# Kernel optimization log

Measured on AMD Instinct MI355X. Metric: run time of the kernel, lower is better.

## Reference

```python
import jax, jax.numpy as jnp
import numpy as np

B, S, D, H = 2, 2048, 1024, 16
DH = D // H          # 64
SP = S // 2          # projected kv length (Linformer)
SCALE = float(np.sqrt(DH))


def setup_inputs() -> dict:
    key = jax.random.key(0)
    ks = jax.random.split(key, 20)
    std = 0.02
    inp = {
        "query": jax.random.normal(ks[0], (B, S, D), jnp.float32),
        "key": jax.random.normal(ks[1], (B, S, D), jnp.float32),
        "value": jax.random.normal(ks[2], (B, S, D), jnp.float32),
        "mask": jax.random.randint(ks[3], (B, 1, 1, S), 0, 2, jnp.int32),
        "Wq": jax.random.normal(ks[4], (D, D), jnp.float32) * std,
        "bq": jnp.zeros((D,), jnp.float32),
        "Wk": jax.random.normal(ks[5], (D, D), jnp.float32) * std,
        "bk": jnp.zeros((D,), jnp.float32),
        "Wv": jax.random.normal(ks[6], (D, D), jnp.float32) * std,
        "bv": jnp.zeros((D,), jnp.float32),
        "Wo": jax.random.normal(ks[7], (D, D), jnp.float32) * std,
        "bo": jnp.zeros((D,), jnp.float32),
        "WkP": jax.random.normal(ks[8], (SP, S), jnp.float32) * std,
        "bkP": jnp.zeros((SP,), jnp.float32),
        "WvP": jax.random.normal(ks[9], (SP, S), jnp.float32) * std,
        "bvP": jnp.zeros((SP,), jnp.float32),
        "apply_proj": 1,
    }
    return inp


def reference(query, key, value, mask, Wq, bq, Wk, bk, Wv, bv, Wo, bo,
              WkP, bkP, WvP, bvP, apply_proj):
    # lin_forward path (apply_proj=True); dropout_ratio=0 -> dropout is identity.
    def heads(x, W, b):  # [B,S,D] -> [B,H,S,DH]
        return (x @ W.T + b).reshape(B, S, H, DH).transpose(0, 2, 1, 3)

    Q = heads(query, Wq, bq)
    K = heads(key, Wk, bk)
    V = heads(value, Wv, bv)

    # masked_fill on transposed [B,H,DH,S] == zero out seq positions
    mseq = (mask != 0).astype(Q.dtype).transpose(0, 1, 3, 2)  # [B,1,S,1]
    Q, K, V = Q * mseq, K * mseq, V * mseq

    # Linformer seq projection S -> SP with exact GELU ('nonlin' config)
    Kp = jax.nn.gelu(jnp.einsum('bhsd,ps->bhpd', K, WkP)
                     + bkP[None, None, :, None], approximate=False)
    Vp = jax.nn.gelu(jnp.einsum('bhsd,ps->bhpd', V, WvP)
                     + bvP[None, None, :, None], approximate=False)

    score = jnp.einsum('bhsd,bhpd->bhsp', Q, Kp) / SCALE   # [B,H,S,SP]
    attn = jax.nn.softmax(score, axis=-1)
    x = jnp.einsum('bhsp,bhpd->bhsd', attn, Vp)            # [B,H,S,DH]
    x = x.transpose(0, 2, 1, 3).reshape(B, S, D)
    return x @ Wo.T + bo
```

## Files before the change

kernel.cpp:

```cpp
#include <hip/hip_runtime.h>
#include <hip/hip_bf16.h>


typedef __attribute__((ext_vector_type(4))) float  f32x4;
typedef __attribute__((ext_vector_type(8))) short  short8;
typedef __attribute__((ext_vector_type(4))) short  short4_t;
typedef __attribute__((ext_vector_type(2))) unsigned int uint32x2;
typedef __attribute__((ext_vector_type(8))) __bf16 bf16x8;
typedef unsigned short ushort_t;

#define DEV __device__ __forceinline__

constexpr int B_ = 2, S_ = 2048, D_ = 1024, H_ = 16, SP_ = 1024;
constexpr size_t M1 = 1u << 20;
constexpr size_t XQ_OFF = 0,      XK_OFF = 4*M1,  XV_OFF = 8*M1,
                 WQ_OFF = 12*M1,  WK_OFF = 13*M1, WV_OFF = 14*M1, WO_OFF = 15*M1,
                 QB_OFF = 4*M1,   KP_OFF = 0,     VPT_OFF = 2*M1,
                 WKPB_OFF = 8*M1, WVPB_OFF = 10*M1, XO_OFF = 8*M1;

DEV ushort_t f2bf(float f) {
  unsigned u = __builtin_bit_cast(unsigned, f);
  unsigned r = ((u >> 16) & 1u) + 0x7FFFu;
  return (ushort_t)((u + r) >> 16);
}
DEV bf16x8 ld8(const ushort_t* p) {
  return __builtin_bit_cast(bf16x8, *reinterpret_cast<const short8*>(p));
}
DEV f32x4 mfma16(bf16x8 a, bf16x8 b, f32x4 c) {
  return __builtin_amdgcn_mfma_f32_16x16x32_bf16(a, b, c, 0, 0, 0);
}
DEV void gload16(const ushort_t* g, ushort_t* l) {
  __builtin_amdgcn_global_load_lds(
      (const __attribute__((address_space(1))) void*)g,
      (__attribute__((address_space(3))) void*)l, 16, 0, 0);
}
DEV void cvt2048(const float* src, ushort_t* dst, int tid) {
  const size_t off = (size_t)tid * 8;
  float4 f0 = *reinterpret_cast<const float4*>(src + off);
  float4 f1 = *reinterpret_cast<const float4*>(src + off + 4);
  ushort_t t[8] = { f2bf(f0.x), f2bf(f0.y), f2bf(f0.z), f2bf(f0.w),
                    f2bf(f1.x), f2bf(f1.y), f2bf(f1.z), f2bf(f1.w) };
  *reinterpret_cast<short8*>(dst + off) = *reinterpret_cast<short8*>(t);
}

__global__ __launch_bounds__(256) void k_convert_a(
    const float* __restrict__ q, const float* __restrict__ k,
    const float* __restrict__ v, const float* __restrict__ Wq,
    const float* __restrict__ Wk, const float* __restrict__ Wv,
    const float* __restrict__ Wo, ushort_t* __restrict__ ws)
{
  int blk = blockIdx.x; const float* src; ushort_t* dst;
  if      (blk < 2048) { src = q;  dst = ws + XQ_OFF; }
  else if (blk < 4096) { src = k;  dst = ws + XK_OFF; blk -= 2048; }
  else if (blk < 6144) { src = v;  dst = ws + XV_OFF; blk -= 4096; }
  else if (blk < 6656) { src = Wq; dst = ws + WQ_OFF; blk -= 6144; }
  else if (blk < 7168) { src = Wk; dst = ws + WK_OFF; blk -= 6656; }
  else if (blk < 7680) { src = Wv; dst = ws + WV_OFF; blk -= 7168; }
  else                 { src = Wo; dst = ws + WO_OFF; blk -= 7680; }
  cvt2048(src + (size_t)blk * 2048, dst + (size_t)blk * 2048, threadIdx.x);
}

__global__ __launch_bounds__(256) void k_convert_b(
    const float* __restrict__ WkP, const float* __restrict__ WvP,
    ushort_t* __restrict__ ws)
{
  int blk = blockIdx.x; const float* src; ushort_t* dst;
  if (blk < 1024) { src = WkP; dst = ws + WKPB_OFF; }
  else            { src = WvP; dst = ws + WVPB_OFF; blk -= 1024; }
  cvt2048(src + (size_t)blk * 2048, dst + (size_t)blk * 2048, threadIdx.x);
}

template<int BIAS, int EPI, int OUTMODE>
DEV void gemmT(const ushort_t* Ap, const ushort_t* Bp, const float* bias,
               const int* mask, void* Cp, int M, int N, int K)
{
  __shared__ __align__(16) ushort_t As[64 * 64];
  __shared__ __align__(16) ushort_t Bs[128 * 64];
  const int tid = threadIdx.x;

  const int gx = gridDim.x, gy = gridDim.y, nwg = gx * gy;
  int lin = blockIdx.y * gx + blockIdx.x;
  lin = (lin & 7) * (nwg >> 3) + (lin >> 3);
  const int m0 = (lin / gy) * 64, n0 = (lin % gy) * 128;

  const int w = tid >> 6, lane = tid & 63, lr = lane & 15, lg = lane >> 4;
  const int wm = (w >> 1) * 32, wn = (w & 1) * 64;
  const int rk7 = lr & 7;

  f32x4 acc[2][4];
#pragma unroll
  for (int i = 0; i < 2; ++i)
#pragma unroll
    for (int j = 0; j < 4; ++j) acc[i][j] = f32x4{0.f, 0.f, 0.f, 0.f};

  const int srow = tid >> 3;
  const int schx = ((tid & 7) ^ (srow & 7)) * 8;
  const ushort_t* Ag = Ap + (size_t)(m0 + srow) * K + schx;
  const ushort_t* Bg = Bp + (size_t)(n0 + srow) * K + schx;

  for (int k0 = 0; k0 < K; k0 += 64) {
    gload16(Ag + k0,                 As + tid*8);
    gload16(Ag + (size_t)32*K + k0,  As + 2048 + tid*8);
    gload16(Bg + k0,                 Bs + tid*8);
    gload16(Bg + (size_t)32*K + k0,  Bs + 2048 + tid*8);
    gload16(Bg + (size_t)64*K + k0,  Bs + 4096 + tid*8);
    gload16(Bg + (size_t)96*K + k0,  Bs + 6144 + tid*8);
    __syncthreads();

#pragma unroll
    for (int ks = 0; ks < 2; ++ks) {
      bf16x8 af[2], bfv[4];
#pragma unroll
      for (int i = 0; i < 2; ++i)
        af[i]  = ld8(&As[(wm + i*16 + lr)*64 + (((ks<<2)|lg) ^ rk7)*8]);
#pragma unroll
      for (int j = 0; j < 4; ++j)
        bfv[j] = ld8(&Bs[(wn + j*16 + lr)*64 + (((ks<<2)|lg) ^ rk7)*8]);
#pragma unroll
      for (int i = 0; i < 2; ++i)
#pragma unroll
        for (int j = 0; j < 4; ++j)
          acc[i][j] = mfma16(af[i], bfv[j], acc[i][j]);
    }
    __syncthreads();
  }

#pragma unroll
  for (int i = 0; i < 2; ++i) {
    const int mBase = m0 + wm + i*16 + 4*lg;
#pragma unroll
    for (int j = 0; j < 4; ++j) {
      const int n = n0 + wn + j*16 + lr;
      float vv[4];
#pragma unroll
      for (int r = 0; r < 4; ++r) {
        const int m = mBase + r;
        float v = acc[i][j][r];
        if (BIAS == 2) v += bias[n];
        if (BIAS == 1) v += bias[m];
        if (EPI == 1)  v = mask[m] ? v : 0.f;
        if (EPI == 2)  v = 0.5f * v * (1.f + erff(v * 0.70710678118654752f));
        vv[r] = v;
      }
      if (OUTMODE == 0) {
#pragma unroll
        for (int r = 0; r < 4; ++r)
          ((ushort_t*)Cp)[(size_t)(mBase + r) * N + n] = f2bf(vv[r]);
      } else if (OUTMODE == 1) {
#pragma unroll
        for (int r = 0; r < 4; ++r)
          ((float*)Cp)[(size_t)(mBase + r) * N + n] = vv[r];
      } else if (OUTMODE == 2) {
        const int bb = mBase >> 11;
        const int sb = mBase & (S_ - 1);
        ushort_t t4[4] = { f2bf(vv[0]), f2bf(vv[1]), f2bf(vv[2]), f2bf(vv[3]) };
        *reinterpret_cast<short4_t*>(
            (ushort_t*)Cp + ((size_t)bb * D_ + n) * S_ + sb) =
            *reinterpret_cast<short4_t*>(t4);
      } else {
        ushort_t t4[4] = { f2bf(vv[0]), f2bf(vv[1]), f2bf(vv[2]), f2bf(vv[3]) };
        *reinterpret_cast<short4_t*>(
            (ushort_t*)Cp + (size_t)n * M + mBase) =
            *reinterpret_cast<short4_t*>(t4);
      }
    }
  }
}

__global__ __launch_bounds__(256) void k_kv(
    const float* __restrict__ bk, const float* __restrict__ bv,
    const int* __restrict__ mask, const ushort_t* __restrict__ ws,
    ushort_t* __restrict__ KbT, ushort_t* __restrict__ VbT)
{
  if (blockIdx.z == 0)
    gemmT<2, 1, 2>(ws + XK_OFF, ws + WK_OFF, bk, mask, KbT, B_*S_, D_, D_);
  else
    gemmT<2, 1, 2>(ws + XV_OFF, ws + WV_OFF, bv, mask, VbT, B_*S_, D_, D_);
}

__global__ __launch_bounds__(256) void k_q(
    const float* __restrict__ bq, const int* __restrict__ mask,
    const ushort_t* __restrict__ ws, ushort_t* __restrict__ Qb)
{
  gemmT<2, 1, 0>(ws + XQ_OFF, ws + WQ_OFF, bq, mask, Qb, B_*S_, D_, D_);
}

__global__ __launch_bounds__(256) void k_linproj(
    const float* __restrict__ bkP, const float* __restrict__ bvP,
    const ushort_t* __restrict__ ws, const ushort_t* __restrict__ KbT,
    const ushort_t* __restrict__ VbT, ushort_t* __restrict__ Kp,
    ushort_t* __restrict__ VpT)
{
  const int z = blockIdx.z, b = z >> 1, isv = z & 1;
  if (isv) {
    gemmT<1, 2, 3>(ws + WVPB_OFF, VbT + (size_t)b * D_ * S_, bvP,
                   nullptr, VpT + (size_t)b * D_ * SP_, SP_, D_, S_);
  } else {
    gemmT<1, 2, 0>(ws + WKPB_OFF, KbT + (size_t)b * D_ * S_, bkP,
                   nullptr, Kp + (size_t)b * SP_ * D_, SP_, D_, S_);
  }
}

__global__ __launch_bounds__(256) void k_outproj(
    const ushort_t* __restrict__ Xo, const ushort_t* __restrict__ Wob,
    const float* __restrict__ bo, float* __restrict__ out)
{
  gemmT<2, 0, 1>(Xo, Wob, bo, nullptr, out, B_*S_, D_, D_);
}

__global__ __launch_bounds__(512) void attn_kernel(
    const ushort_t* __restrict__ Qb, const ushort_t* __restrict__ Kp,
    const ushort_t* __restrict__ VpT, ushort_t* __restrict__ Xo)
{
  __shared__ __align__(16) ushort_t Ks[2][64 * 64];
  __shared__ __align__(16) ushort_t Vs[2][64 * 64];
  __shared__ __align__(16) ushort_t Pl[8][16][72];

  const int b = blockIdx.z, h = blockIdx.y, s0 = blockIdx.x * 128;
  const int tid = threadIdx.x, w = tid >> 6, lane = tid & 63;
  const int lr = lane & 15, lg = lane >> 4;

  const ushort_t* qp = Qb + (size_t)(b * S_ + s0 + w*16 + lr) * D_ + h * 64;
  const bf16x8 aq0 = ld8(qp + 8*lg);
  const bf16x8 aq1 = ld8(qp + 32 + 8*lg);

  const ushort_t* kbase = Kp  + (size_t)b * SP_ * D_ + h * 64;
  const ushort_t* vbase = VpT + (size_t)b * D_ * SP_ + (size_t)(h*64) * SP_;

  const int srow = tid >> 3, sch = tid & 7;
  const int schx = (sch ^ (srow & 7)) << 3;

  f32x4 o[4];
#pragma unroll
  for (int dt = 0; dt < 4; ++dt) o[dt] = f32x4{0.f, 0.f, 0.f, 0.f};
  float lsum4[4] = {0.f, 0.f, 0.f, 0.f};
  constexpr float C_ = 0.18033688011112042f;

  gload16(kbase + (size_t)srow * D_ + schx, Ks[0] + tid*8);
  gload16(vbase + (size_t)srow * SP_ + schx, Vs[0] + tid*8);
  __syncthreads();

  int cur = 0;
  for (int pt = 0; pt < SP_ / 64; ++pt) {
    if (pt + 1 < SP_ / 64) {
      const int p1 = (pt + 1) * 64;
      gload16(kbase + (size_t)(p1 + srow) * D_ + schx, Ks[cur^1] + tid*8);
      gload16(vbase + (size_t)srow * SP_ + p1 + schx, Vs[cur^1] + tid*8);
    }

    const int rk7 = lr & 7;
#pragma unroll
    for (int nt = 0; nt < 4; ++nt) {
      const ushort_t* krow = Ks[cur] + (nt*16 + lr) * 64;
      f32x4 a = f32x4{0.f, 0.f, 0.f, 0.f};
      a = mfma16(ld8(krow + ((lg       ^ rk7) << 3)), aq0, a);
      a = mfma16(ld8(krow + (((4 + lg) ^ rk7) << 3)), aq1, a);
      const float e0 = __builtin_exp2f(a[0] * C_);
      const float e1 = __builtin_exp2f(a[1] * C_);
      const float e2 = __builtin_exp2f(a[2] * C_);
      const float e3 = __builtin_exp2f(a[3] * C_);
      lsum4[nt] += (e0 + e1) + (e2 + e3);
      unsigned p01, p23;
      asm("v_cvt_pk_bf16_f32 %0, %1, %2" : "=v"(p01) : "v"(e0), "v"(e1));
      asm("v_cvt_pk_bf16_f32 %0, %1, %2" : "=v"(p23) : "v"(e2), "v"(e3));
      uint32x2 pw; pw[0] = p01; pw[1] = p23;
      *reinterpret_cast<uint32x2*>(&Pl[w][lr][nt*16 + 4*lg]) = pw;
    }

    const bf16x8 pa0 = ld8(&Pl[w][lr][8*lg]);
    const bf16x8 pa1 = ld8(&Pl[w][lr][32 + 8*lg]);
#pragma unroll
    for (int dt = 0; dt < 4; ++dt) {
      const ushort_t* vrow = Vs[cur] + (dt*16 + lr) * 64;
      o[dt] = mfma16(pa0, ld8(vrow + ((lg       ^ rk7) << 3)), o[dt]);
      o[dt] = mfma16(pa1, ld8(vrow + (((4 + lg) ^ rk7) << 3)), o[dt]);
    }

    __syncthreads();
    cur ^= 1;
  }

  float lsum = (lsum4[0] + lsum4[1]) + (lsum4[2] + lsum4[3]);
  lsum += __shfl_xor(lsum, 16, 64);
  lsum += __shfl_xor(lsum, 32, 64);
  float linv[4];
#pragma unroll
  for (int r = 0; r < 4; ++r)
    linv[r] = 1.f / __shfl(lsum, 4*lg + r, 64);

#pragma unroll
  for (int dt = 0; dt < 4; ++dt)
#pragma unroll
    for (int r = 0; r < 4; ++r) {
      const int srow2 = s0 + w*16 + 4*lg + r;
      Xo[(size_t)(b * S_ + srow2) * D_ + h*64 + dt*16 + lr] =
          f2bf(o[dt][r] * linv[r]);
    }
}

extern "C" void kernel_launch(void* const* d_in, const int* in_sizes, int n_in,
                              void* d_out, int out_size, void* d_ws, size_t ws_size,
                              hipStream_t stream)
{
  const float* q   = (const float*)d_in[0];
  const float* k   = (const float*)d_in[1];
  const float* v   = (const float*)d_in[2];
  const int*   msk = (const int*)d_in[3];
  const float* Wq  = (const float*)d_in[4];
  const float* bq  = (const float*)d_in[5];
  const float* Wk  = (const float*)d_in[6];
  const float* bk  = (const float*)d_in[7];
  const float* Wv  = (const float*)d_in[8];
  const float* bv  = (const float*)d_in[9];
  const float* Wo  = (const float*)d_in[10];
  const float* bo  = (const float*)d_in[11];
  const float* WkP = (const float*)d_in[12];
  const float* bkP = (const float*)d_in[13];
  const float* WvP = (const float*)d_in[14];
  const float* bvP = (const float*)d_in[15];

  ushort_t* ws  = (ushort_t*)d_ws;
  ushort_t* Qb  = ws + QB_OFF;
  ushort_t* Kp  = ws + KP_OFF;
  ushort_t* VpT = ws + VPT_OFF;
  ushort_t* Xo  = ws + XO_OFF;
  ushort_t* KbT = (ushort_t*)d_out;
  ushort_t* VbT = KbT + 4 * M1;

  dim3 blk(256, 1, 1);
  k_convert_a<<<dim3(8192, 1, 1), blk, 0, stream>>>(q, k, v, Wq, Wk, Wv, Wo, ws);
  k_kv     <<<dim3(B_*S_/64, D_/128, 2), blk, 0, stream>>>(bk, bv, msk, ws, KbT, VbT);
  k_q      <<<dim3(B_*S_/64, D_/128, 1), blk, 0, stream>>>(bq, msk, ws, Qb);
  k_convert_b<<<dim3(2048, 1, 1), blk, 0, stream>>>(WkP, WvP, ws);
  k_linproj<<<dim3(SP_/64,  D_/128, 4), blk, 0, stream>>>(bkP, bvP, ws, KbT, VbT, Kp, VpT);
  attn_kernel<<<dim3(S_/128, H_, B_), dim3(512,1,1), 0, stream>>>(Qb, Kp, VpT, Xo);
  k_outproj<<<dim3(B_*S_/64, D_/128, 1), blk, 0, stream>>>(Xo, ws + WO_OFF, bo, (float*)d_out);
}
```

Before: 148.5 us.

## Process two query groups per attention block and fold softmax scale into Q

The attention kernel now handles 256 query rows per block, two 128-row groups, and loads each K/V tile's fragments from LDS once into registers for reuse by both groups. This halves K/V global loads and LDS traffic per query row. The softmax scale constant is multiplied into Q in the Q-projection epilogue, so the exp2 in the inner loop no longer needs a multiply. The costs are half as many blocks (256 vs 512), more registers per thread under a launch-bounds hint of two blocks, and Q stored in bf16 after scaling, which adds a small rounding difference.

```diff
diff --git a/kernel.cpp b/kernel.cpp
--- a/kernel.cpp
+++ b/kernel.cpp
@@ -17,6 +17,7 @@
                  WQ_OFF = 12*M1,  WK_OFF = 13*M1, WV_OFF = 14*M1, WO_OFF = 15*M1,
                  QB_OFF = 4*M1,   KP_OFF = 0,     VPT_OFF = 2*M1,
                  WKPB_OFF = 8*M1, WVPB_OFF = 10*M1, XO_OFF = 8*M1;
+constexpr float CSC = 0.18033688011112042f;
 
 DEV ushort_t f2bf(float f) {
   unsigned u = __builtin_bit_cast(unsigned, f);
@@ -138,7 +139,8 @@
         float v = acc[i][j][r];
         if (BIAS == 2) v += bias[n];
         if (BIAS == 1) v += bias[m];
-        if (EPI == 1)  v = mask[m] ? v : 0.f;
+        if (EPI == 1 || EPI == 3) v = mask[m] ? v : 0.f;
+        if (EPI == 3)  v *= CSC;
         if (EPI == 2)  v = 0.5f * v * (1.f + erff(v * 0.70710678118654752f));
         vv[r] = v;
       }
@@ -182,7 +184,7 @@
     const float* __restrict__ bq, const int* __restrict__ mask,
     const ushort_t* __restrict__ ws, ushort_t* __restrict__ Qb)
 {
-  gemmT<2, 1, 0>(ws + XQ_OFF, ws + WQ_OFF, bq, mask, Qb, B_*S_, D_, D_);
+  gemmT<2, 3, 0>(ws + XQ_OFF, ws + WQ_OFF, bq, mask, Qb, B_*S_, D_, D_);
 }
 
 __global__ __launch_bounds__(256) void k_linproj(
@@ -208,7 +210,7 @@
   gemmT<2, 0, 1>(Xo, Wob, bo, nullptr, out, B_*S_, D_, D_);
 }
 
-__global__ __launch_bounds__(512) void attn_kernel(
+__global__ __launch_bounds__(512, 2) void attn_kernel(
     const ushort_t* __restrict__ Qb, const ushort_t* __restrict__ Kp,
     const ushort_t* __restrict__ VpT, ushort_t* __restrict__ Xo)
 {
@@ -216,25 +218,32 @@
   __shared__ __align__(16) ushort_t Vs[2][64 * 64];
   __shared__ __align__(16) ushort_t Pl[8][16][72];
 
-  const int b = blockIdx.z, h = blockIdx.y, s0 = blockIdx.x * 128;
+  const int b = blockIdx.z, h = blockIdx.y, s0 = blockIdx.x * 256;
   const int tid = threadIdx.x, w = tid >> 6, lane = tid & 63;
   const int lr = lane & 15, lg = lane >> 4;
 
-  const ushort_t* qp = Qb + (size_t)(b * S_ + s0 + w*16 + lr) * D_ + h * 64;
-  const bf16x8 aq0 = ld8(qp + 8*lg);
-  const bf16x8 aq1 = ld8(qp + 32 + 8*lg);
+  bf16x8 aq[2][2];
+#pragma unroll
+  for (int g = 0; g < 2; ++g) {
+    const ushort_t* qp =
+        Qb + (size_t)(b * S_ + s0 + g*128 + w*16 + lr) * D_ + h * 64;
+    aq[g][0] = ld8(qp + 8*lg);
+    aq[g][1] = ld8(qp + 32 + 8*lg);
+  }
 
   const ushort_t* kbase = Kp  + (size_t)b * SP_ * D_ + h * 64;
   const ushort_t* vbase = VpT + (size_t)b * D_ * SP_ + (size_t)(h*64) * SP_;
 
   const int srow = tid >> 3, sch = tid & 7;
   const int schx = (sch ^ (srow & 7)) << 3;
-
-  f32x4 o[4];
-#pragma unroll
-  for (int dt = 0; dt < 4; ++dt) o[dt] = f32x4{0.f, 0.f, 0.f, 0.f};
-  float lsum4[4] = {0.f, 0.f, 0.f, 0.f};
-  constexpr float C_ = 0.18033688011112042f;
+  const int rk7 = lr & 7;
+
+  f32x4 o[2][4];
+#pragma unroll
+  for (int g = 0; g < 2; ++g)
+#pragma unroll
+    for (int dt = 0; dt < 4; ++dt) o[g][dt] = f32x4{0.f, 0.f, 0.f, 0.f};
+  float lsum4[2][4] = {};
 
   gload16(kbase + (size_t)srow * D_ + schx, Ks[0] + tid*8);
   gload16(vbase + (size_t)srow * SP_ + schx, Vs[0] + tid*8);
@@ -248,54 +257,66 @@
       gload16(vbase + (size_t)srow * SP_ + p1 + schx, Vs[cur^1] + tid*8);
     }
 
-    const int rk7 = lr & 7;
+    bf16x8 kf[4][2], vf[4][2];
 #pragma unroll
     for (int nt = 0; nt < 4; ++nt) {
       const ushort_t* krow = Ks[cur] + (nt*16 + lr) * 64;
-      f32x4 a = f32x4{0.f, 0.f, 0.f, 0.f};
-      a = mfma16(ld8(krow + ((lg       ^ rk7) << 3)), aq0, a);
-      a = mfma16(ld8(krow + (((4 + lg) ^ rk7) << 3)), aq1, a);
-      const float e0 = __builtin_exp2f(a[0] * C_);
-      const float e1 = __builtin_exp2f(a[1] * C_);
-      const float e2 = __builtin_exp2f(a[2] * C_);
-      const float e3 = __builtin_exp2f(a[3] * C_);
-      lsum4[nt] += (e0 + e1) + (e2 + e3);
-      unsigned p01, p23;
-      asm("v_cvt_pk_bf16_f32 %0, %1, %2" : "=v"(p01) : "v"(e0), "v"(e1));
-      asm("v_cvt_pk_bf16_f32 %0, %1, %2" : "=v"(p23) : "v"(e2), "v"(e3));
-      uint32x2 pw; pw[0] = p01; pw[1] = p23;
-      *reinterpret_cast<uint32x2*>(&Pl[w][lr][nt*16 + 4*lg]) = pw;
-    }
-
-    const bf16x8 pa0 = ld8(&Pl[w][lr][8*lg]);
-    const bf16x8 pa1 = ld8(&Pl[w][lr][32 + 8*lg]);
-#pragma unroll
-    for (int dt = 0; dt < 4; ++dt) {
-      const ushort_t* vrow = Vs[cur] + (dt*16 + lr) * 64;
-      o[dt] = mfma16(pa0, ld8(vrow + ((lg       ^ rk7) << 3)), o[dt]);
-      o[dt] = mfma16(pa1, ld8(vrow + (((4 + lg) ^ rk7) << 3)), o[dt]);
+      kf[nt][0] = ld8(krow + ((lg       ^ rk7) << 3));
+      kf[nt][1] = ld8(krow + (((4 + lg) ^ rk7) << 3));
+      const ushort_t* vrow = Vs[cur] + (nt*16 + lr) * 64;
+      vf[nt][0] = ld8(vrow + ((lg       ^ rk7) << 3));
+      vf[nt][1] = ld8(vrow + (((4 + lg) ^ rk7) << 3));
+    }
+
+#pragma unroll
+    for (int g = 0; g < 2; ++g) {
+#pragma unroll
+      for (int nt = 0; nt < 4; ++nt) {
+        f32x4 a = f32x4{0.f, 0.f, 0.f, 0.f};
+        a = mfma16(kf[nt][0], aq[g][0], a);
+        a = mfma16(kf[nt][1], aq[g][1], a);
+        const float e0 = __builtin_exp2f(a[0]);
+        const float e1 = __builtin_exp2f(a[1]);
+        const float e2 = __builtin_exp2f(a[2]);
+        const float e3 = __builtin_exp2f(a[3]);
+        lsum4[g][nt] += (e0 + e1) + (e2 + e3);
+        unsigned p01, p23;
+        asm("v_cvt_pk_bf16_f32 %0, %1, %2" : "=v"(p01) : "v"(e0), "v"(e1));
+        asm("v_cvt_pk_bf16_f32 %0, %1, %2" : "=v"(p23) : "v"(e2), "v"(e3));
+        uint32x2 pw; pw[0] = p01; pw[1] = p23;
+        *reinterpret_cast<uint32x2*>(&Pl[w][lr][nt*16 + 4*lg]) = pw;
+      }
+      const bf16x8 pa0 = ld8(&Pl[w][lr][8*lg]);
+      const bf16x8 pa1 = ld8(&Pl[w][lr][32 + 8*lg]);
+#pragma unroll
+      for (int dt = 0; dt < 4; ++dt) {
+        o[g][dt] = mfma16(pa0, vf[dt][0], o[g][dt]);
+        o[g][dt] = mfma16(pa1, vf[dt][1], o[g][dt]);
+      }
     }
 
     __syncthreads();
     cur ^= 1;
   }
 
-  float lsum = (lsum4[0] + lsum4[1]) + (lsum4[2] + lsum4[3]);
-  lsum += __shfl_xor(lsum, 16, 64);
-  lsum += __shfl_xor(lsum, 32, 64);
-  float linv[4];
-#pragma unroll
-  for (int r = 0; r < 4; ++r)
-    linv[r] = 1.f / __shfl(lsum, 4*lg + r, 64);
-
-#pragma unroll
-  for (int dt = 0; dt < 4; ++dt)
-#pragma unroll
-    for (int r = 0; r < 4; ++r) {
-      const int srow2 = s0 + w*16 + 4*lg + r;
-      Xo[(size_t)(b * S_ + srow2) * D_ + h*64 + dt*16 + lr] =
-          f2bf(o[dt][r] * linv[r]);
-    }
+#pragma unroll
+  for (int g = 0; g < 2; ++g) {
+    float lsum = (lsum4[g][0] + lsum4[g][1]) + (lsum4[g][2] + lsum4[g][3]);
+    lsum += __shfl_xor(lsum, 16, 64);
+    lsum += __shfl_xor(lsum, 32, 64);
+    float linv[4];
+#pragma unroll
+    for (int r = 0; r < 4; ++r)
+      linv[r] = 1.f / __shfl(lsum, 4*lg + r, 64);
+#pragma unroll
+    for (int dt = 0; dt < 4; ++dt)
+#pragma unroll
+      for (int r = 0; r < 4; ++r) {
+        const int srow2 = s0 + g*128 + w*16 + 4*lg + r;
+        Xo[(size_t)(b * S_ + srow2) * D_ + h*64 + dt*16 + lr] =
+            f2bf(o[g][dt][r] * linv[r]);
+      }
+  }
 }
 
 extern "C" void kernel_launch(void* const* d_in, const int* in_sizes, int n_in,
@@ -333,6 +354,6 @@
   k_q      <<<dim3(B_*S_/64, D_/128, 1), blk, 0, stream>>>(bq, msk, ws, Qb);
   k_convert_b<<<dim3(2048, 1, 1), blk, 0, stream>>>(WkP, WvP, ws);
   k_linproj<<<dim3(SP_/64,  D_/128, 4), blk, 0, stream>>>(bkP, bvP, ws, KbT, VbT, Kp, VpT);
-  attn_kernel<<<dim3(S_/128, H_, B_), dim3(512,1,1), 0, stream>>>(Qb, Kp, VpT, Xo);
+  attn_kernel<<<dim3(S_/256, H_, B_), dim3(512,1,1), 0, stream>>>(Qb, Kp, VpT, Xo);
   k_outproj<<<dim3(B_*S_/64, D_/128, 1), blk, 0, stream>>>(Xo, ws + WO_OFF, bo, (float*)d_out);
 }
```

New measurement: 149.2 us. No clear change (+0.4%).

## Double-buffer GEMM LDS tiles and fold softmax scale into Q projection

Applied to the files above, without the earlier changes.

The shared GEMM template now uses two LDS buffers, prefetching the next K tile with global_load_lds while the current one is consumed. Partial vmcnt waits and raw s_barrier replace the full __syncthreads. The attention kernel gets the same explicit waitcnt/barrier pipelining. The softmax scale (log2e/sqrt(dh)) is folded into the Q projection epilogue, which removes one multiply per score. The cost is twice the GEMM LDS footprint, which may reduce occupancy, and Q is rounded to bf16 after scaling, which slightly changes precision.

```diff
diff --git a/kernel.cpp b/kernel.cpp
--- a/kernel.cpp
+++ b/kernel.cpp
@@ -17,6 +17,7 @@
                  WQ_OFF = 12*M1,  WK_OFF = 13*M1, WV_OFF = 14*M1, WO_OFF = 15*M1,
                  QB_OFF = 4*M1,   KP_OFF = 0,     VPT_OFF = 2*M1,
                  WKPB_OFF = 8*M1, WVPB_OFF = 10*M1, XO_OFF = 8*M1;
+constexpr float CSC = 0.18033688011112042f;
 
 DEV ushort_t f2bf(float f) {
   unsigned u = __builtin_bit_cast(unsigned, f);
@@ -74,8 +75,8 @@
 DEV void gemmT(const ushort_t* Ap, const ushort_t* Bp, const float* bias,
                const int* mask, void* Cp, int M, int N, int K)
 {
-  __shared__ __align__(16) ushort_t As[64 * 64];
-  __shared__ __align__(16) ushort_t Bs[128 * 64];
+  __shared__ __align__(16) ushort_t As[2][64 * 64];
+  __shared__ __align__(16) ushort_t Bs[2][128 * 64];
   const int tid = threadIdx.x;
 
   const int gx = gridDim.x, gy = gridDim.y, nwg = gx * gy;
@@ -98,31 +99,46 @@
   const ushort_t* Ag = Ap + (size_t)(m0 + srow) * K + schx;
   const ushort_t* Bg = Bp + (size_t)(n0 + srow) * K + schx;
 
+  auto stage = [&](int buf, int k0) {
+    gload16(Ag + k0,                 As[buf] + tid*8);
+    gload16(Ag + (size_t)32*K + k0,  As[buf] + 2048 + tid*8);
+    gload16(Bg + k0,                 Bs[buf] + tid*8);
+    gload16(Bg + (size_t)32*K + k0,  Bs[buf] + 2048 + tid*8);
+    gload16(Bg + (size_t)64*K + k0,  Bs[buf] + 4096 + tid*8);
+    gload16(Bg + (size_t)96*K + k0,  Bs[buf] + 6144 + tid*8);
+  };
+
+  stage(0, 0);
+  int cur = 0;
   for (int k0 = 0; k0 < K; k0 += 64) {
-    gload16(Ag + k0,                 As + tid*8);
-    gload16(Ag + (size_t)32*K + k0,  As + 2048 + tid*8);
-    gload16(Bg + k0,                 Bs + tid*8);
-    gload16(Bg + (size_t)32*K + k0,  Bs + 2048 + tid*8);
-    gload16(Bg + (size_t)64*K + k0,  Bs + 4096 + tid*8);
-    gload16(Bg + (size_t)96*K + k0,  Bs + 6144 + tid*8);
-    __syncthreads();
+    if (k0 + 64 < K) {
+      stage(cur ^ 1, k0 + 64);
+      asm volatile("s_waitcnt vmcnt(6)" ::: "memory");
+    } else {
+      asm volatile("s_waitcnt vmcnt(0)" ::: "memory");
+    }
+    __builtin_amdgcn_s_barrier();
+    __builtin_amdgcn_sched_barrier(0);
 
 #pragma unroll
     for (int ks = 0; ks < 2; ++ks) {
       bf16x8 af[2], bfv[4];
 #pragma unroll
       for (int i = 0; i < 2; ++i)
-        af[i]  = ld8(&As[(wm + i*16 + lr)*64 + (((ks<<2)|lg) ^ rk7)*8]);
+        af[i]  = ld8(&As[cur][(wm + i*16 + lr)*64 + (((ks<<2)|lg) ^ rk7)*8]);
 #pragma unroll
       for (int j = 0; j < 4; ++j)
-        bfv[j] = ld8(&Bs[(wn + j*16 + lr)*64 + (((ks<<2)|lg) ^ rk7)*8]);
+        bfv[j] = ld8(&Bs[cur][(wn + j*16 + lr)*64 + (((ks<<2)|lg) ^ rk7)*8]);
 #pragma unroll
       for (int i = 0; i < 2; ++i)
 #pragma unroll
         for (int j = 0; j < 4; ++j)
           acc[i][j] = mfma16(af[i], bfv[j], acc[i][j]);
     }
-    __syncthreads();
+
+    __builtin_amdgcn_sched_barrier(0);
+    __builtin_amdgcn_s_barrier();
+    cur ^= 1;
   }
 
 #pragma unroll
@@ -138,7 +154,8 @@
         float v = acc[i][j][r];
         if (BIAS == 2) v += bias[n];
         if (BIAS == 1) v += bias[m];
-        if (EPI == 1)  v = mask[m] ? v : 0.f;
+        if (EPI == 1 || EPI == 3) v = mask[m] ? v : 0.f;
+        if (EPI == 3)  v *= CSC;
         if (EPI == 2)  v = 0.5f * v * (1.f + erff(v * 0.70710678118654752f));
         vv[r] = v;
       }
@@ -182,7 +199,7 @@
     const float* __restrict__ bq, const int* __restrict__ mask,
     const ushort_t* __restrict__ ws, ushort_t* __restrict__ Qb)
 {
-  gemmT<2, 1, 0>(ws + XQ_OFF, ws + WQ_OFF, bq, mask, Qb, B_*S_, D_, D_);
+  gemmT<2, 3, 0>(ws + XQ_OFF, ws + WQ_OFF, bq, mask, Qb, B_*S_, D_, D_);
 }
 
 __global__ __launch_bounds__(256) void k_linproj(
@@ -229,36 +246,40 @@
 
   const int srow = tid >> 3, sch = tid & 7;
   const int schx = (sch ^ (srow & 7)) << 3;
+  const int rk7 = lr & 7;
 
   f32x4 o[4];
 #pragma unroll
   for (int dt = 0; dt < 4; ++dt) o[dt] = f32x4{0.f, 0.f, 0.f, 0.f};
   float lsum4[4] = {0.f, 0.f, 0.f, 0.f};
-  constexpr float C_ = 0.18033688011112042f;
-
-  gload16(kbase + (size_t)srow * D_ + schx, Ks[0] + tid*8);
-  gload16(vbase + (size_t)srow * SP_ + schx, Vs[0] + tid*8);
-  __syncthreads();
-
+
+  auto stage = [&](int buf, int p0) {
+    gload16(kbase + (size_t)(p0 + srow) * D_ + schx, Ks[buf] + tid*8);
+    gload16(vbase + (size_t)srow * SP_ + p0 + schx,  Vs[buf] + tid*8);
+  };
+
+  stage(0, 0);
   int cur = 0;
   for (int pt = 0; pt < SP_ / 64; ++pt) {
     if (pt + 1 < SP_ / 64) {
-      const int p1 = (pt + 1) * 64;
-      gload16(kbase + (size_t)(p1 + srow) * D_ + schx, Ks[cur^1] + tid*8);
-      gload16(vbase + (size_t)srow * SP_ + p1 + schx, Vs[cur^1] + tid*8);
-    }
-
-    const int rk7 = lr & 7;
+      stage(cur ^ 1, (pt + 1) * 64);
+      asm volatile("s_waitcnt vmcnt(2)" ::: "memory");
+    } else {
+      asm volatile("s_waitcnt vmcnt(0)" ::: "memory");
+    }
+    __builtin_amdgcn_s_barrier();
+    __builtin_amdgcn_sched_barrier(0);
+
 #pragma unroll
     for (int nt = 0; nt < 4; ++nt) {
       const ushort_t* krow = Ks[cur] + (nt*16 + lr) * 64;
       f32x4 a = f32x4{0.f, 0.f, 0.f, 0.f};
       a = mfma16(ld8(krow + ((lg       ^ rk7) << 3)), aq0, a);
       a = mfma16(ld8(krow + (((4 + lg) ^ rk7) << 3)), aq1, a);
-      const float e0 = __builtin_exp2f(a[0] * C_);
-      const float e1 = __builtin_exp2f(a[1] * C_);
-      const float e2 = __builtin_exp2f(a[2] * C_);
-      const float e3 = __builtin_exp2f(a[3] * C_);
+      const float e0 = __builtin_exp2f(a[0]);
+      const float e1 = __builtin_exp2f(a[1]);
+      const float e2 = __builtin_exp2f(a[2]);
+      const float e3 = __builtin_exp2f(a[3]);
       lsum4[nt] += (e0 + e1) + (e2 + e3);
       unsigned p01, p23;
       asm("v_cvt_pk_bf16_f32 %0, %1, %2" : "=v"(p01) : "v"(e0), "v"(e1));
@@ -276,7 +297,8 @@
       o[dt] = mfma16(pa1, ld8(vrow + (((4 + lg) ^ rk7) << 3)), o[dt]);
     }
 
-    __syncthreads();
+    __builtin_amdgcn_sched_barrier(0);
+    __builtin_amdgcn_s_barrier();
     cur ^= 1;
   }
 
```

Result: slower. 173.5 us (+16.8%).
